# Kernel tuning notes

Measured on AMD Instinct MI355X. Metric: run time of the kernel, lower is better.

Reference implementation:

```python
import jax, jax.numpy as jnp
import numpy as np

DIM = 256
HEADS = 8
DIM_HEAD = 64
INNER = HEADS * DIM_HEAD  # 512
SCALE = DIM_HEAD ** -0.5


def setup_inputs() -> dict:
    key = jax.random.key(0)
    ks = jax.random.split(key, 6)
    b, n, m = 8, 2048, 16
    x = jax.random.normal(ks[0], (b, n, DIM), dtype=jnp.float32)
    y = jax.random.normal(ks[1], (b, n, m, DIM), dtype=jnp.float32)
    # nn.Linear weights stored as [out, in] in torch; we use [in, out] for x @ W
    W_q = jax.random.normal(ks[2], (DIM, INNER), dtype=jnp.float32) * (DIM ** -0.5)
    W_kv = jax.random.normal(ks[3], (DIM, 2 * INNER), dtype=jnp.float32) * (DIM ** -0.5)
    W_out = jax.random.normal(ks[4], (INNER, DIM), dtype=jnp.float32) * (INNER ** -0.5)
    b_out = jax.random.normal(ks[5], (DIM,), dtype=jnp.float32) * 0.01
    return {"x": x, "y": y, "W_q": W_q, "W_kv": W_kv, "W_out": W_out, "b_out": b_out}


def reference(x, y, W_q, W_kv, W_out, b_out):
    b, n, m, _ = y.shape
    h, d = HEADS, DIM_HEAD
    q = (x @ W_q).reshape(b, n, h, d)                      # [b,n,h,d] (single query per position)
    kv = y @ W_kv                                          # [b,n,m,2*inner]
    k, v = jnp.split(kv, 2, axis=-1)
    k = k.reshape(b, n, m, h, d)
    v = v.reshape(b, n, m, h, d)
    dots = jnp.einsum('bnhd,bnmhd->bnhm', q, k) * SCALE    # scores over m context tokens
    attn = jax.nn.softmax(dots, axis=-1)
    out = jnp.einsum('bnhm,bnmhd->bnhd', attn, v).reshape(b, n, h * d)
    return out @ W_out + b_out                             # [b,n,dim]
```

## Files before the change

### kernel.cpp

```cpp
#include <hip/hip_runtime.h>
#include <cmath>

#define NPOS 16384
#define ATT_SCALE 0.125f

typedef float f4 __attribute__((ext_vector_type(4)));
typedef short short8 __attribute__((ext_vector_type(8)));
typedef unsigned int uint;
typedef unsigned short ushort;

__device__ __forceinline__ ushort f2bf(float f) {
    union { float f; uint u; } v; v.f = f;
    uint r = v.u + 0x7fffu + ((v.u >> 16) & 1u);
    return (ushort)(r >> 16);
}
__device__ __forceinline__ float bfl(uint u) { union { uint u; float f; } v; v.u = u << 16; return v.f; }
__device__ __forceinline__ float bfh(uint u) { union { uint u; float f; } v; v.u = u & 0xffff0000u; return v.f; }

__device__ __forceinline__ void gl_lds16(const ushort* g, ushort* l) {
    __builtin_amdgcn_global_load_lds(
        (const __attribute__((address_space(1))) uint*)g,
        (__attribute__((address_space(3))) uint*)l, 16, 0, 0);
}

template<int BN, bool C_F32, bool BIAS>
__global__ __launch_bounds__(256) void gemm_bt(
    const ushort* __restrict__ A, int lda,
    const ushort* __restrict__ Bt, int ldb,
    void* __restrict__ Cg, int ldc,
    const float* __restrict__ bias, int K)
{
    constexpr int NSUB = BN / 16;
    __shared__ __align__(16) ushort A_lds[128 * 32];
    __shared__ __align__(16) ushort B_lds[BN * 32];
    const int mt = blockIdx.x, nt = blockIdx.y;
    const int row0 = mt * 128, col0 = nt * BN;
    const int tid = threadIdx.x;
    const int lane = tid & 63, w = tid >> 6;
    const int frow = lane & 15, quad = lane >> 4;
    const int lrow = lane >> 2, lk = (lane & 3) * 8;

    f4 acc[2][NSUB];
    #pragma unroll
    for (int mi = 0; mi < 2; ++mi)
        #pragma unroll
        for (int ni = 0; ni < NSUB; ++ni)
            acc[mi][ni] = (f4){0.f, 0.f, 0.f, 0.f};

    for (int k0 = 0; k0 < K; k0 += 32) {
        #pragma unroll
        for (int it = 0; it < 2; ++it) {
            int start = w * 16 + it * 64;
            gl_lds16(A + (size_t)(row0 + start + lrow) * lda + k0 + lk,
                     &A_lds[start * 32]);
        }
        #pragma unroll
        for (int it = 0; it < BN / 64; ++it) {
            int start = w * 16 + it * 64;
            gl_lds16(Bt + (size_t)(col0 + start + lrow) * ldb + k0 + lk,
                     &B_lds[start * 32]);
        }
        __syncthreads();

        short8 a0 = *(const short8*)&A_lds[(w * 32 + frow) * 32 + quad * 8];
        short8 a1 = *(const short8*)&A_lds[(w * 32 + 16 + frow) * 32 + quad * 8];
        #pragma unroll
        for (int ni = 0; ni < NSUB; ++ni) {
            short8 b = *(const short8*)&B_lds[(ni * 16 + frow) * 32 + quad * 8];
            acc[0][ni] = __builtin_amdgcn_mfma_f32_16x16x32_bf16(b, a0, acc[0][ni], 0, 0, 0);
            acc[1][ni] = __builtin_amdgcn_mfma_f32_16x16x32_bf16(b, a1, acc[1][ni], 0, 0, 0);
        }
        __syncthreads();
    }

    #pragma unroll
    for (int mi = 0; mi < 2; ++mi) {
        const int r = row0 + w * 32 + mi * 16 + frow;
        #pragma unroll
        for (int ni = 0; ni < NSUB; ++ni) {
            const int c = col0 + ni * 16 + quad * 4;
            f4 v = acc[mi][ni];
            if (C_F32) {
                float* C = (float*)Cg;
                if (BIAS) {
                    const float4 bv = *(const float4*)&bias[c];
                    v[0] += bv.x; v[1] += bv.y; v[2] += bv.z; v[3] += bv.w;
                }
                *(float4*)&C[(size_t)r * ldc + c] = make_float4(v[0], v[1], v[2], v[3]);
            } else {
                ushort* C = (ushort*)Cg;
                uint2 pv;
                pv.x = (uint)f2bf(v[0]) | ((uint)f2bf(v[1]) << 16);
                pv.y = (uint)f2bf(v[2]) | ((uint)f2bf(v[3]) << 16);
                *(uint2*)&C[(size_t)r * ldc + c] = pv;
            }
        }
    }
}

__global__ __launch_bounds__(256) void prep_all(
    const float* __restrict__ x, ushort* __restrict__ xb,
    const float* __restrict__ Wq, const float* __restrict__ Wkv,
    const float* __restrict__ Wout,
    ushort* __restrict__ Wf1n, ushort* __restrict__ Wf2t)
{
    __shared__ float As[64][65];
    __shared__ float Bs[64][65];

    if (blockIdx.x >= 256) {
        const int i = ((blockIdx.x - 256) * 256 + threadIdx.x) * 8;
        float4 v0 = *(const float4*)&x[i];
        float4 v1 = *(const float4*)&x[i + 4];
        uint4 p;
        p.x = (uint)f2bf(v0.x) | ((uint)f2bf(v0.y) << 16);
        p.y = (uint)f2bf(v0.z) | ((uint)f2bf(v0.w) << 16);
        p.z = (uint)f2bf(v1.x) | ((uint)f2bf(v1.y) << 16);
        p.w = (uint)f2bf(v1.z) | ((uint)f2bf(v1.w) << 16);
        *(uint4*)&xb[i] = p;
        return;
    }

    const int b = blockIdx.x;
    const bool second = (b >= 128);
    const int bb = second ? b - 128 : b;
    const int h = bb >> 4, ct = (bb >> 2) & 3, et = bb & 3;
    const int t = threadIdx.x;
    const int c0 = ct * 64, e0 = et * 64;
    const int tx = t & 15, ty = t >> 4;

    const float* Ab = Wkv + (second ? 512 : 0) + h * 64;
    #pragma unroll
    for (int it = 0; it < 4; ++it) {
        int idx = t + it * 256;
        int row = idx >> 4, col = (idx & 15) * 4;
        float4 v = *(const float4*)&Ab[(size_t)(c0 + row) * 1024 + col];
        As[row][col] = v.x; As[row][col + 1] = v.y;
        As[row][col + 2] = v.z; As[row][col + 3] = v.w;
    }
    #pragma unroll
    for (int it = 0; it < 4; ++it) {
        int idx = t + it * 256;
        int row = idx >> 4, col = (idx & 15) * 4;
        float4 v;
        if (second)
            v = *(const float4*)&Wout[(size_t)(h * 64 + row) * 256 + e0 + col];
        else
            v = *(const float4*)&Wq[(size_t)(e0 + row) * 512 + h * 64 + col];
        Bs[row][col] = v.x; Bs[row][col + 1] = v.y;
        Bs[row][col + 2] = v.z; Bs[row][col + 3] = v.w;
    }
    __syncthreads();

    float acc[4][4] = {};
    if (!second) {
        for (int k = 0; k < 64; ++k) {
            float a[4], bb2[4];
            #pragma unroll
            for (int i = 0; i < 4; ++i) a[i] = As[ty * 4 + i][k];
            #pragma unroll
            for (int j = 0; j < 4; ++j) bb2[j] = Bs[tx * 4 + j][k];
            #pragma unroll
            for (int i = 0; i < 4; ++i)
                #pragma unroll
                for (int j = 0; j < 4; ++j)
                    acc[i][j] = fmaf(a[i], bb2[j], acc[i][j]);
        }
        #pragma unroll
        for (int i = 0; i < 4; ++i) {
            int c = c0 + ty * 4 + i;
            uint2 pv;
            pv.x = (uint)f2bf(acc[i][0]) | ((uint)f2bf(acc[i][1]) << 16);
            pv.y = (uint)f2bf(acc[i][2]) | ((uint)f2bf(acc[i][3]) << 16);
            *(uint2*)&Wf1n[(size_t)(h * 256 + c) * 256 + e0 + tx * 4] = pv;
        }
    } else {
        for (int k = 0; k < 64; ++k) {
            float a[4], bb2[4];
            #pragma unroll
            for (int j = 0; j < 4; ++j) a[j] = As[tx * 4 + j][k];
            #pragma unroll
            for (int i = 0; i < 4; ++i) bb2[i] = Bs[k][ty * 4 + i];
            #pragma unroll
            for (int i = 0; i < 4; ++i)
                #pragma unroll
                for (int j = 0; j < 4; ++j)
                    acc[i][j] = fmaf(bb2[i], a[j], acc[i][j]);
        }
        #pragma unroll
        for (int i = 0; i < 4; ++i) {
            int e = e0 + ty * 4 + i;
            uint2 pv;
            pv.x = (uint)f2bf(acc[i][0]) | ((uint)f2bf(acc[i][1]) << 16);
            pv.y = (uint)f2bf(acc[i][2]) | ((uint)f2bf(acc[i][3]) << 16);
            *(uint2*)&Wf2t[(size_t)e * 2048 + h * 256 + c0 + tx * 4] = pv;
        }
    }
}

__global__ __launch_bounds__(256) void attn_k(
    const float* __restrict__ y, ushort* __restrict__ qk)
{
    __shared__ float ylds[16 * 260];
    __shared__ float qkf[8 * 260];
    __shared__ float part[4][8][16];
    __shared__ __align__(16) float attn_sT[16][8];
    const int p = blockIdx.x;
    const int t = threadIdx.x;
    const int w = t >> 6, lane = t & 63;
    const float* yp = y + (size_t)p * 4096;
    ushort* qkp = qk + (size_t)p * 2048;

    #pragma unroll
    for (int it = 0; it < 4; ++it) {
        int i = t + it * 256;
        float4 v = ((const float4*)yp)[i];
        int m = i >> 6, c4 = (i & 63) * 4;
        *(float4*)&ylds[m * 260 + c4] = v;
    }
    #pragma unroll
    for (int it = 0; it < 2; ++it) {
        int i = t + it * 256;
        uint2 v = ((const uint2*)qkp)[i];
        int h = i >> 6, c4 = (i & 63) * 4;
        float4 f = make_float4(bfl(v.x), bfh(v.x), bfl(v.y), bfh(v.y));
        *(float4*)&qkf[h * 260 + c4] = f;
    }
    __syncthreads();

    {
        const int m = t & 15, cs = t >> 4;
        float ps[8] = {0.f, 0.f, 0.f, 0.f, 0.f, 0.f, 0.f, 0.f};
        #pragma unroll
        for (int jj = 0; jj < 4; ++jj) {
            float4 yv = *(const float4*)&ylds[m * 260 + cs * 16 + jj * 4];
            #pragma unroll
            for (int h = 0; h < 8; ++h) {
                float4 qv = *(const float4*)&qkf[h * 260 + cs * 16 + jj * 4];
                ps[h] += yv.x * qv.x + yv.y * qv.y + yv.z * qv.z + yv.w * qv.w;
            }
        }
        #pragma unroll
        for (int h = 0; h < 8; ++h) {
            float s = ps[h];
            s += __shfl_xor(s, 16);
            s += __shfl_xor(s, 32);
            if (lane < 16) part[w][h][m] = s;
        }
    }
    __syncthreads();

    if (t < 128) {
        const int h = t >> 4, mm = t & 15;
        float d = (part[0][h][mm] + part[1][h][mm] + part[2][h][mm] + part[3][h][mm]) * ATT_SCALE;
        float mx = d;
        #pragma unroll
        for (int off = 8; off >= 1; off >>= 1) mx = fmaxf(mx, __shfl_xor(mx, off));
        float e = __expf(d - mx);
        float sm = e;
        #pragma unroll
        for (int off = 8; off >= 1; off >>= 1) sm += __shfl_xor(sm, off);
        attn_sT[mm][h] = e / sm;
    }
    __syncthreads();

    {
        float acc[8] = {0.f, 0.f, 0.f, 0.f, 0.f, 0.f, 0.f, 0.f};
        #pragma unroll
        for (int mm = 0; mm < 16; ++mm) {
            float yv = ylds[mm * 260 + t];
            float4 a0 = *(const float4*)&attn_sT[mm][0];
            float4 a1 = *(const float4*)&attn_sT[mm][4];
            acc[0] = fmaf(a0.x, yv, acc[0]);
            acc[1] = fmaf(a0.y, yv, acc[1]);
            acc[2] = fmaf(a0.z, yv, acc[2]);
            acc[3] = fmaf(a0.w, yv, acc[3]);
            acc[4] = fmaf(a1.x, yv, acc[4]);
            acc[5] = fmaf(a1.y, yv, acc[5]);
            acc[6] = fmaf(a1.z, yv, acc[6]);
            acc[7] = fmaf(a1.w, yv, acc[7]);
        }
        #pragma unroll
        for (int h = 0; h < 8; ++h) qkp[h * 256 + t] = f2bf(acc[h]);
    }
}

extern "C" void kernel_launch(void* const* d_in, const int* in_sizes, int n_in,
                              void* d_out, int out_size, void* d_ws, size_t ws_size,
                              hipStream_t stream)
{
    (void)in_sizes; (void)n_in; (void)out_size; (void)ws_size;
    const float* x     = (const float*)d_in[0];
    const float* y     = (const float*)d_in[1];
    const float* W_q   = (const float*)d_in[2];
    const float* W_kv  = (const float*)d_in[3];
    const float* W_out = (const float*)d_in[4];
    const float* b_out = (const float*)d_in[5];
    float* out = (float*)d_out;

    ushort* qk   = (ushort*)d_ws;
    ushort* xb   = qk + (size_t)NPOS * 2048;
    ushort* Wf1n = xb + (size_t)NPOS * 256;
    ushort* Wf2t = Wf1n + 2048 * 256;

    dim3 blk(256);

    prep_all<<<dim3(2304), blk, 0, stream>>>(x, xb, W_q, W_kv, W_out, Wf1n, Wf2t);

    gemm_bt<128, false, false><<<dim3(128, 16), blk, 0, stream>>>(
        xb, 256, Wf1n, 256, qk, 2048, nullptr, 256);

    attn_k<<<dim3(NPOS), blk, 0, stream>>>(y, qk);

    gemm_bt<64, true, true><<<dim3(128, 4), blk, 0, stream>>>(
        qk, 2048, Wf2t, 2048, out, 256, b_out, 2048);
}
```

Before: 483.5 us.

## Use 2x2 warp tiling, K=64 steps and XOR-swizzled LDS in bf16 GEMM

Restructures the GEMM so each of the four waves computes a 64 x BN/2 sub-tile instead of a 32 x BN strip. This reuses A and B fragments across several MFMAs and cuts LDS reads per MFMA. The K step doubles to 64, halving the number of barriers, and an XOR swizzle on the 16-byte chunks is meant to avoid LDS bank conflicts. In exchange it doubles LDS use per block and raises accumulator register pressure, which may lower occupancy.

```diff
diff --git a/kernel.cpp b/kernel.cpp
--- a/kernel.cpp
+++ b/kernel.cpp
@@ -30,55 +30,64 @@
     void* __restrict__ Cg, int ldc,
     const float* __restrict__ bias, int K)
 {
-    constexpr int NSUB = BN / 16;
-    __shared__ __align__(16) ushort A_lds[128 * 32];
-    __shared__ __align__(16) ushort B_lds[BN * 32];
+    constexpr int NI = BN / 32;
+    __shared__ __align__(16) ushort A_lds[128 * 64];
+    __shared__ __align__(16) ushort B_lds[BN * 64];
     const int mt = blockIdx.x, nt = blockIdx.y;
     const int row0 = mt * 128, col0 = nt * BN;
     const int tid = threadIdx.x;
     const int lane = tid & 63, w = tid >> 6;
     const int frow = lane & 15, quad = lane >> 4;
-    const int lrow = lane >> 2, lk = (lane & 3) * 8;
-
-    f4 acc[2][NSUB];
-    #pragma unroll
-    for (int mi = 0; mi < 2; ++mi)
-        #pragma unroll
-        for (int ni = 0; ni < NSUB; ++ni)
+    const int wr = (w >> 1) * 64, wc = (w & 1) * (BN / 2);
+    const int srow = lane >> 3;
+    const int gch = ((lane & 7) ^ (lane >> 3)) * 8;
+
+    f4 acc[4][NI];
+    #pragma unroll
+    for (int mi = 0; mi < 4; ++mi)
+        #pragma unroll
+        for (int ni = 0; ni < NI; ++ni)
             acc[mi][ni] = (f4){0.f, 0.f, 0.f, 0.f};
 
-    for (int k0 = 0; k0 < K; k0 += 32) {
-        #pragma unroll
-        for (int it = 0; it < 2; ++it) {
-            int start = w * 16 + it * 64;
-            gl_lds16(A + (size_t)(row0 + start + lrow) * lda + k0 + lk,
-                     &A_lds[start * 32]);
-        }
-        #pragma unroll
-        for (int it = 0; it < BN / 64; ++it) {
-            int start = w * 16 + it * 64;
-            gl_lds16(Bt + (size_t)(col0 + start + lrow) * ldb + k0 + lk,
-                     &B_lds[start * 32]);
+    for (int k0 = 0; k0 < K; k0 += 64) {
+        #pragma unroll
+        for (int it = 0; it < 4; ++it) {
+            int sr = (it * 4 + w) * 8;
+            gl_lds16(A + (size_t)(row0 + sr + srow) * lda + k0 + gch,
+                     &A_lds[sr * 64]);
+        }
+        #pragma unroll
+        for (int it = 0; it < BN / 32; ++it) {
+            int sr = (it * 4 + w) * 8;
+            gl_lds16(Bt + (size_t)(col0 + sr + srow) * ldb + k0 + gch,
+                     &B_lds[sr * 64]);
         }
         __syncthreads();
 
-        short8 a0 = *(const short8*)&A_lds[(w * 32 + frow) * 32 + quad * 8];
-        short8 a1 = *(const short8*)&A_lds[(w * 32 + 16 + frow) * 32 + quad * 8];
-        #pragma unroll
-        for (int ni = 0; ni < NSUB; ++ni) {
-            short8 b = *(const short8*)&B_lds[(ni * 16 + frow) * 32 + quad * 8];
-            acc[0][ni] = __builtin_amdgcn_mfma_f32_16x16x32_bf16(b, a0, acc[0][ni], 0, 0, 0);
-            acc[1][ni] = __builtin_amdgcn_mfma_f32_16x16x32_bf16(b, a1, acc[1][ni], 0, 0, 0);
+        #pragma unroll
+        for (int kk = 0; kk < 2; ++kk) {
+            const int ko = (((kk * 4 + quad) ^ (frow & 7)) << 3);
+            short8 av[4];
+            #pragma unroll
+            for (int mi = 0; mi < 4; ++mi)
+                av[mi] = *(const short8*)&A_lds[(wr + mi * 16 + frow) * 64 + ko];
+            #pragma unroll
+            for (int ni = 0; ni < NI; ++ni) {
+                short8 bv = *(const short8*)&B_lds[(wc + ni * 16 + frow) * 64 + ko];
+                #pragma unroll
+                for (int mi = 0; mi < 4; ++mi)
+                    acc[mi][ni] = __builtin_amdgcn_mfma_f32_16x16x32_bf16(bv, av[mi], acc[mi][ni], 0, 0, 0);
+            }
         }
         __syncthreads();
     }
 
     #pragma unroll
-    for (int mi = 0; mi < 2; ++mi) {
-        const int r = row0 + w * 32 + mi * 16 + frow;
-        #pragma unroll
-        for (int ni = 0; ni < NSUB; ++ni) {
-            const int c = col0 + ni * 16 + quad * 4;
+    for (int mi = 0; mi < 4; ++mi) {
+        const int r = row0 + wr + mi * 16 + frow;
+        #pragma unroll
+        for (int ni = 0; ni < NI; ++ni) {
+            const int c = col0 + wc + ni * 16 + quad * 4;
             f4 v = acc[mi][ni];
             if (C_F32) {
                 float* C = (float*)Cg;
```

Result: faster. 466.6 us, median of 2 (-3.5%).
